# Performance work log

Hardware: AMD Instinct MI355X
Metric: run time of the kernel (lower is better)

## Reference

```python
import jax, jax.numpy as jnp
import numpy as np

B, A, D = 256, 128, 5          # batch, max_atoms, max_degree
FA, FB, C = 256, 64, 256       # atom feats, bond feats, conv_width


def setup_inputs() -> dict:
    key = jax.random.key(0)
    k1, k2, k3, k4 = jax.random.split(key, 4)
    atoms = jax.random.normal(k1, (B, A, FA), dtype=jnp.float32)
    bonds = jax.random.normal(k2, (B, A, D, FB), dtype=jnp.float32)
    # neighbour indices with -1 as padding value
    edges = jax.random.randint(k3, (B, A, D), -1, A, dtype=jnp.int32)
    W = jax.random.normal(k4, (D, FA + FB, C), dtype=jnp.float32) * 0.05
    b = jnp.zeros((D, C), dtype=jnp.float32)
    return {"atoms": atoms, "bonds": bonds, "edges": edges, "W": W, "b": b}


def reference(atoms, bonds, edges, W, b):
    # atom degree = number of non-padding neighbours  (B, A)
    deg = jnp.sum(edges != -1, axis=-1)

    # neighbour_lookup: pad a zero atom at index 0, shift indices by +1 so -1 -> 0
    masked_atoms = jnp.pad(atoms, ((0, 0), (1, 0), (0, 0)))        # (B, A+1, FA)
    idx = edges + 1                                                # (B, A, D)
    neigh = masked_atoms[jnp.arange(B)[:, None, None], idx]        # (B, A, D, FA)

    # include_self=True then sum over neighbour axis == self + sum(neighbours)
    summed_atom = atoms + jnp.sum(neigh, axis=2)                   # (B, A, FA)
    summed_bond = jnp.sum(bonds, axis=2)                           # (B, A, FB)
    feat = jnp.concatenate([summed_atom, summed_bond], axis=-1)    # (B, A, FA+FB)

    # per-degree Dense (relu), masked by (degree == d), summed over degrees
    dense = jax.nn.relu(jnp.einsum('baf,dfc->badc', feat, W) + b)  # (B, A, D, C)
    mask = (deg[..., None] == jnp.arange(D)).astype(dense.dtype)   # (B, A, D)
    return jnp.einsum('badc,bad->bac', dense, mask)                # (B, A, C)
```

## Files before the change

kernel.cpp:

```cpp
#include <hip/hip_runtime.h>


#define ND 5
#define NA 128
#define NFA 256
#define NFB 64
#define NC 256
#define NF 320
#define RPB 16
#define NBLK 2048

__device__ __forceinline__ float bcast(float v, int l) {
    return __int_as_float(__builtin_amdgcn_readlane(__float_as_int(v), l));
}

__global__ __launch_bounds__(256) void ngh_kernel(
    const float* __restrict__ atoms,
    const float* __restrict__ bonds,
    const int*   __restrict__ edges,
    const float* __restrict__ W,
    const float* __restrict__ bias,
    float* __restrict__ out)
{
    const int t     = threadIdx.x;
    const int lane  = t & 63;
    const int wv    = t >> 6;
    const int rbase = blockIdx.x * RPB;

    __shared__ int edges_s[RPB * ND];
    __shared__ int deg_s[RPB];

    if (t < RPB * ND) edges_s[t] = edges[rbase * ND + t];
    __syncthreads();

    if (t < RPB) {
        int deg = 0;
#pragma unroll
        for (int dd = 0; dd < ND; ++dd)
            deg += (edges_s[t * ND + dd] != -1) ? 1 : 0;
        deg_s[t] = deg;
    }
    __syncthreads();

    {
        float4* out4 = (float4*)out + (size_t)rbase * (NC / 4);
#pragma unroll
        for (int k = 0; k < RPB * (NC / 4) / 256; ++k) {
            const int i = t + 256 * k;
            if (deg_s[i >> 6] == ND)
                out4[i] = make_float4(0.f, 0.f, 0.f, 0.f);
        }
    }

    int h = 0;
    for (int rl = 0; rl < RPB; ++rl) {
        const int d = deg_s[rl];
        if (d >= ND) continue;
        if ((h++ & 3) != wv) continue;

        const int row = rbase + rl;
        const int bb  = row >> 7;

        const int e0 = edges_s[rl * ND + 0];
        const int e1 = edges_s[rl * ND + 1];
        const int e2 = edges_s[rl * ND + 2];
        const int e3 = edges_s[rl * ND + 3];
        const int e4 = edges_s[rl * ND + 4];

        const float* arow = atoms + (size_t)row * NFA;
        float f0 = arow[      lane];
        float f1 = arow[ 64 + lane];
        float f2 = arow[128 + lane];
        float f3 = arow[192 + lane];
#define ADD_NEIGH(E)                                                       \
        if ((E) >= 0) {                                                    \
            const float* nr = atoms + (size_t)(bb * NA + (E)) * NFA;       \
            f0 += nr[      lane];                                          \
            f1 += nr[ 64 + lane];                                          \
            f2 += nr[128 + lane];                                          \
            f3 += nr[192 + lane];                                          \
        }
        ADD_NEIGH(e0) ADD_NEIGH(e1) ADD_NEIGH(e2) ADD_NEIGH(e3) ADD_NEIGH(e4)
#undef ADD_NEIGH
        float fb = 0.f;
#pragma unroll
        for (int dd = 0; dd < ND; ++dd)
            fb += bonds[((size_t)row * ND + dd) * NFB + lane];

        const float4* W4 = (const float4*)W + (size_t)d * NF * (NC / 4) + lane;
        float4 acc = ((const float4*)bias)[d * (NC / 4) + lane];

#define FMA_CHUNK(FREG, FBASE)                                             \
        _Pragma("unroll 16")                                               \
        for (int l = 0; l < 64; ++l) {                                     \
            const float  s = bcast((FREG), l);                             \
            const float4 w = W4[(size_t)((FBASE) + l) * (NC / 4)];         \
            acc.x = fmaf(s, w.x, acc.x);                                   \
            acc.y = fmaf(s, w.y, acc.y);                                   \
            acc.z = fmaf(s, w.z, acc.z);                                   \
            acc.w = fmaf(s, w.w, acc.w);                                   \
        }
        FMA_CHUNK(f0,   0)
        FMA_CHUNK(f1,  64)
        FMA_CHUNK(f2, 128)
        FMA_CHUNK(f3, 192)
        FMA_CHUNK(fb, 256)
#undef FMA_CHUNK

        ((float4*)out)[(size_t)row * (NC / 4) + lane] =
            make_float4(fmaxf(acc.x, 0.f), fmaxf(acc.y, 0.f),
                        fmaxf(acc.z, 0.f), fmaxf(acc.w, 0.f));
    }
}

extern "C" void kernel_launch(void* const* d_in, const int* in_sizes, int n_in,
                              void* d_out, int out_size, void* d_ws, size_t ws_size,
                              hipStream_t stream) {
    const float* atoms = (const float*)d_in[0];
    const float* bonds = (const float*)d_in[1];
    const int*   edges = (const int*)  d_in[2];
    const float* W     = (const float*)d_in[3];
    const float* bias  = (const float*)d_in[4];
    float*       out   = (float*)d_out;

    ngh_kernel<<<NBLK, 256, 0, stream>>>(atoms, bonds, edges, W, bias, out);
}
```

Before: 137.5 us.

## Split each row's dot product across four waves with shared-memory reduction

Each row is now handled by all four waves of the block instead of one wave. Each wave reduces an 80-feature slice of the input against W, and the partial sums are combined through shared memory with double-buffered feature and partial staging. The change also halves rows per block, doubles the grid, adds an occupancy hint, and uses nontemporal stores for output. The aim is to remove load imbalance and the per-row serial readlane work of the old one-row-per-wave mapping. In exchange it adds two block barriers per row and LDS traffic.

Result: no change. 136.5 us (-0.7%).

```diff
diff --git a/kernel.cpp b/kernel.cpp
--- a/kernel.cpp
+++ b/kernel.cpp
@@ -7,14 +7,12 @@
 #define NFB 64
 #define NC 256
 #define NF 320
-#define RPB 16
-#define NBLK 2048
+#define RPB 8
+#define NBLK 4096
 
-__device__ __forceinline__ float bcast(float v, int l) {
-    return __int_as_float(__builtin_amdgcn_readlane(__float_as_int(v), l));
-}
+typedef float vf4 __attribute__((ext_vector_type(4)));
 
-__global__ __launch_bounds__(256) void ngh_kernel(
+__global__ __launch_bounds__(256, 4) void ngh_kernel(
     const float* __restrict__ atoms,
     const float* __restrict__ bonds,
     const int*   __restrict__ edges,
@@ -27,12 +25,13 @@
     const int wv    = t >> 6;
     const int rbase = blockIdx.x * RPB;
 
-    __shared__ int edges_s[RPB * ND];
-    __shared__ int deg_s[RPB];
+    __shared__ int   edges_s[RPB * ND];
+    __shared__ int   deg_s[RPB];
+    __shared__ float feat[2][NF];
+    __shared__ vf4   psum[2][3][64];
 
     if (t < RPB * ND) edges_s[t] = edges[rbase * ND + t];
     __syncthreads();
-
     if (t < RPB) {
         int deg = 0;
 #pragma unroll
@@ -42,74 +41,73 @@
     }
     __syncthreads();
 
+    int p = 0;
+    for (int rl = 0; rl < RPB; ++rl) {
+        const int d = deg_s[rl];
+        if (d >= ND) continue;
+        const int row = rbase + rl;
+        const int bb  = row >> 7;
+
+        {
+            float v = atoms[(size_t)row * NFA + t];
+#pragma unroll
+            for (int dd = 0; dd < ND; ++dd) {
+                const int e = edges_s[rl * ND + dd];
+                if (e >= 0)
+                    v += atoms[(size_t)(bb * NA + e) * NFA + t];
+            }
+            feat[p][t] = v;
+            if (t < NFB) {
+                float s = 0.f;
+#pragma unroll
+                for (int dd = 0; dd < ND; ++dd)
+                    s += bonds[((size_t)row * ND + dd) * NFB + t];
+                feat[p][NFA + t] = s;
+            }
+        }
+        __syncthreads();
+
+        const vf4* fseg = (const vf4*)(feat[p] + 80 * wv);
+        const vf4* W4   = (const vf4*)W +
+                          ((size_t)d * NF + 80 * wv) * (NC / 4) + lane;
+        vf4 a = {0.f, 0.f, 0.f, 0.f};
+#pragma unroll 4
+        for (int fc = 0; fc < 20; ++fc) {
+            const vf4 fv = fseg[fc];
+            const vf4 w0 = W4[(fc * 4 + 0) * 64];
+            const vf4 w1 = W4[(fc * 4 + 1) * 64];
+            const vf4 w2 = W4[(fc * 4 + 2) * 64];
+            const vf4 w3 = W4[(fc * 4 + 3) * 64];
+            a += fv.x * w0;
+            a += fv.y * w1;
+            a += fv.z * w2;
+            a += fv.w * w3;
+        }
+        if (wv > 0) psum[p][wv - 1][lane] = a;
+        __syncthreads();
+
+        if (wv == 0) {
+            vf4 r = a + psum[p][0][lane] + psum[p][1][lane] + psum[p][2][lane]
+                      + ((const vf4*)bias)[d * (NC / 4) + lane];
+            r.x = fmaxf(r.x, 0.f);
+            r.y = fmaxf(r.y, 0.f);
+            r.z = fmaxf(r.z, 0.f);
+            r.w = fmaxf(r.w, 0.f);
+            __builtin_nontemporal_store(
+                r, (vf4*)out + (size_t)row * (NC / 4) + lane);
+        }
+        p ^= 1;
+    }
+
     {
-        float4* out4 = (float4*)out + (size_t)rbase * (NC / 4);
+        vf4* out4 = (vf4*)out + (size_t)rbase * (NC / 4);
+        const vf4 z = {0.f, 0.f, 0.f, 0.f};
 #pragma unroll
         for (int k = 0; k < RPB * (NC / 4) / 256; ++k) {
             const int i = t + 256 * k;
             if (deg_s[i >> 6] == ND)
-                out4[i] = make_float4(0.f, 0.f, 0.f, 0.f);
+                __builtin_nontemporal_store(z, &out4[i]);
         }
-    }
-
-    int h = 0;
-    for (int rl = 0; rl < RPB; ++rl) {
-        const int d = deg_s[rl];
-        if (d >= ND) continue;
-        if ((h++ & 3) != wv) continue;
-
-        const int row = rbase + rl;
-        const int bb  = row >> 7;
-
-        const int e0 = edges_s[rl * ND + 0];
-        const int e1 = edges_s[rl * ND + 1];
-        const int e2 = edges_s[rl * ND + 2];
-        const int e3 = edges_s[rl * ND + 3];
-        const int e4 = edges_s[rl * ND + 4];
-
-        const float* arow = atoms + (size_t)row * NFA;
-        float f0 = arow[      lane];
-        float f1 = arow[ 64 + lane];
-        float f2 = arow[128 + lane];
-        float f3 = arow[192 + lane];
-#define ADD_NEIGH(E)                                                       \
-        if ((E) >= 0) {                                                    \
-            const float* nr = atoms + (size_t)(bb * NA + (E)) * NFA;       \
-            f0 += nr[      lane];                                          \
-            f1 += nr[ 64 + lane];                                          \
-            f2 += nr[128 + lane];                                          \
-            f3 += nr[192 + lane];                                          \
-        }
-        ADD_NEIGH(e0) ADD_NEIGH(e1) ADD_NEIGH(e2) ADD_NEIGH(e3) ADD_NEIGH(e4)
-#undef ADD_NEIGH
-        float fb = 0.f;
-#pragma unroll
-        for (int dd = 0; dd < ND; ++dd)
-            fb += bonds[((size_t)row * ND + dd) * NFB + lane];
-
-        const float4* W4 = (const float4*)W + (size_t)d * NF * (NC / 4) + lane;
-        float4 acc = ((const float4*)bias)[d * (NC / 4) + lane];
-
-#define FMA_CHUNK(FREG, FBASE)                                             \
-        _Pragma("unroll 16")                                               \
-        for (int l = 0; l < 64; ++l) {                                     \
-            const float  s = bcast((FREG), l);                             \
-            const float4 w = W4[(size_t)((FBASE) + l) * (NC / 4)];         \
-            acc.x = fmaf(s, w.x, acc.x);                                   \
-            acc.y = fmaf(s, w.y, acc.y);                                   \
-            acc.z = fmaf(s, w.z, acc.z);                                   \
-            acc.w = fmaf(s, w.w, acc.w);                                   \
-        }
-        FMA_CHUNK(f0,   0)
-        FMA_CHUNK(f1,  64)
-        FMA_CHUNK(f2, 128)
-        FMA_CHUNK(f3, 192)
-        FMA_CHUNK(fb, 256)
-#undef FMA_CHUNK
-
-        ((float4*)out)[(size_t)row * (NC / 4) + lane] =
-            make_float4(fmaxf(acc.x, 0.f), fmaxf(acc.y, 0.f),
-                        fmaxf(acc.z, 0.f), fmaxf(acc.w, 0.f));
     }
 }
 
```
